# Performance work log

Hardware: AMD Instinct MI355X
Metric: run time of the kernel (lower is better)

Reference implementation:

```python
import jax, jax.numpy as jnp
import numpy as np

N_NODES = 100000
N_EDGES = 1000000
IN_CH = 128
HID = 128
N_CLS = 3


def setup_inputs() -> dict:
    key = jax.random.key(0)
    ks = jax.random.split(key, 10)
    scale_in = 1.0 / np.sqrt(IN_CH)
    scale_h = 1.0 / np.sqrt(HID)
    return {
        "x": jax.random.normal(ks[0], (N_NODES, IN_CH), dtype=jnp.float32),
        "edge_index": jax.random.randint(ks[1], (2, N_EDGES), 0, N_NODES, dtype=jnp.int64),
        # SAGEConv layer 1: lin_l (aggregated neighbors, with bias), lin_r (root, no bias)
        "w_l1": jax.random.normal(ks[2], (IN_CH, HID), dtype=jnp.float32) * scale_in,
        "b_l1": jnp.zeros((HID,), dtype=jnp.float32),
        "w_r1": jax.random.normal(ks[3], (IN_CH, HID), dtype=jnp.float32) * scale_in,
        # SAGEConv layer 2
        "w_l2": jax.random.normal(ks[4], (HID, HID), dtype=jnp.float32) * scale_h,
        "b_l2": jnp.zeros((HID,), dtype=jnp.float32),
        "w_r2": jax.random.normal(ks[5], (HID, HID), dtype=jnp.float32) * scale_h,
        # final classifier
        "w_cls": jax.random.normal(ks[6], (HID, N_CLS), dtype=jnp.float32) * scale_h,
        "b_cls": jnp.zeros((N_CLS,), dtype=jnp.float32),
    }


def _sage_conv(x, src, dst, w_l, b_l, w_r, num_nodes):
    # mean aggregation of source-node features onto destination nodes
    msg = x[src]                                              # [E, C] gather
    agg = jax.ops.segment_sum(msg, dst, num_segments=num_nodes)
    cnt = jax.ops.segment_sum(jnp.ones((src.shape[0],), x.dtype), dst,
                              num_segments=num_nodes)
    mean = agg / jnp.maximum(cnt, 1.0)[:, None]
    # out = lin_l(mean_aggr) + lin_r(x)
    return mean @ w_l + b_l + x @ w_r


def reference(x, edge_index, w_l1, b_l1, w_r1, w_l2, b_l2, w_r2, w_cls, b_cls):
    src, dst = edge_index[0], edge_index[1]
    n = x.shape[0]
    h = jax.nn.relu(_sage_conv(x, src, dst, w_l1, b_l1, w_r1, n))
    # dropout is identity in eval mode
    h = jax.nn.relu(_sage_conv(h, src, dst, w_l2, b_l2, w_r2, n))
    logits = h @ w_cls + b_cls
    return logits
```

## Files before the change

### kernel.cpp

```cpp
#include <hip/hip_runtime.h>
#include <hip/hip_bf16.h>

#define N_NODES 100000
#define N_EDGES 1000000
#define CH 128
#define KTOT 256
#define NCLS 3

#define NBKT 196
#define EPB 4096
#define NB_A ((N_EDGES + EPB - 1) / EPB)
#define M_H (NBKT * NB_A)
#define CHK ((M_H + 1023) / 1024)

#define NB_CVTX (N_NODES * CH / 4 / 256)
#define NB_CVTW (KTOT * CH / 256)
#define NB_A1 (NB_A + NB_CVTX + 2 * NB_CVTW)

typedef __attribute__((ext_vector_type(8))) short v8s;
typedef __attribute__((ext_vector_type(4))) float v4f;

__device__ __forceinline__ float bf2f(unsigned short u) {
    return __uint_as_float(((unsigned int)u) << 16);
}

__device__ __forceinline__ unsigned short f2bf(float f) {
    unsigned int u = __float_as_uint(f);
    unsigned int r = (u + 0x7fffu + ((u >> 16) & 1u)) >> 16;
    return (unsigned short)r;
}

__device__ __forceinline__ int edge_at(const void* e, int is64, long long i) {
    if (is64) return (int)((const long long*)e)[i];
    return ((const int*)e)[i];
}

__device__ __forceinline__ float ldf(const void* p, int isbf, size_t i) {
    if (isbf) return bf2f(((const unsigned short*)p)[i]);
    return ((const float*)p)[i];
}

__device__ __forceinline__ void acc_u32(unsigned int u, float& a0, float& a1) {
    a0 += bf2f((unsigned short)(u & 0xffffu));
    a1 += bf2f((unsigned short)(u >> 16));
}

__global__ void k_init(const void* __restrict__ e, const unsigned int* __restrict__ x,
                       int* __restrict__ eflag, int* __restrict__ dtf) {
    if (blockIdx.x == 0) {
        if (threadIdx.x < 64) {
            int v = ((const int*)e)[2 * threadIdx.x + 1];
            unsigned long long bl = __ballot(v != 0);
            if (threadIdx.x == 0) *eflag = (bl == 0ULL) ? 1 : 0;
        }
    } else {
        if (threadIdx.x < 64) {
            unsigned int u = x[threadIdx.x];
            int ex = (u >> 7) & 0xff;
            int sane = (ex == 0) || (ex >= 100 && ex <= 154);
            unsigned long long bl = __ballot(sane);
            if (threadIdx.x == 0) *dtf = (__popcll(bl) >= 48) ? 1 : 0;
        }
    }
}

__global__ void k_A1(const void* __restrict__ e, const int* __restrict__ eflag,
                     const int* __restrict__ dtf, int* __restrict__ hist,
                     const void* __restrict__ x, unsigned short* __restrict__ Abuf,
                     const void* __restrict__ wl1, const void* __restrict__ wr1,
                     unsigned short* __restrict__ WT1,
                     const void* __restrict__ wl2, const void* __restrict__ wr2,
                     unsigned short* __restrict__ WT2) {
    int b = blockIdx.x;
    int t = threadIdx.x;
    if (b < NB_A) {
        __shared__ int h[NBKT];
        if (t < NBKT) h[t] = 0;
        __syncthreads();
        int is64 = *eflag;
#pragma unroll
        for (int j = 0; j < EPB / 256; j++) {
            int i = b * EPB + j * 256 + t;
            if (i < N_EDGES) {
                int dst = edge_at(e, is64, (long long)N_EDGES + i);
                atomicAdd(&h[dst >> 9], 1);
            }
        }
        __syncthreads();
        if (t < NBKT) hist[t * NB_A + b] = h[t];
    } else {
        int ob = b - NB_A;
        if (ob < NB_CVTX) {
            int idx = ob * 256 + t;
            int node = idx >> 5;
            int ch = (idx & 31) * 4;
            int isbf = *dtf;
            unsigned short o[4];
            if (isbf) {
                ushort4 u = *(const ushort4*)((const unsigned short*)x +
                                              (size_t)node * CH + ch);
                o[0] = u.x; o[1] = u.y; o[2] = u.z; o[3] = u.w;
            } else {
                float4 v = *(const float4*)((const float*)x + (size_t)node * CH + ch);
                o[0] = f2bf(v.x); o[1] = f2bf(v.y); o[2] = f2bf(v.z); o[3] = f2bf(v.w);
            }
            *(ushort4*)(Abuf + (size_t)node * KTOT + CH + ch) =
                make_ushort4(o[0], o[1], o[2], o[3]);
        } else {
            int rel = ob - NB_CVTX;
            const void* wl = (rel < NB_CVTW) ? wl1 : wl2;
            const void* wr = (rel < NB_CVTW) ? wr1 : wr2;
            unsigned short* WT = (rel < NB_CVTW) ? WT1 : WT2;
            int i = (rel % NB_CVTW) * 256 + t;
            int k = i >> 7;
            int n = i & 127;
            int isbf = *dtf;
            float v = (k < CH) ? ldf(wl, isbf, (size_t)k * CH + n)
                               : ldf(wr, isbf, (size_t)(k - CH) * CH + n);
            WT[(size_t)n * KTOT + k] = f2bf(v);
        }
    }
}

__global__ __launch_bounds__(1024) void k_scanH(int* __restrict__ hist,
                                                int* __restrict__ bktbase) {
    __shared__ int ps[1024];
    int t = threadIdx.x;
    int lv[CHK];
    int s = 0;
    int base0 = t * CHK;
#pragma unroll
    for (int j = 0; j < CHK; j++) {
        int idx = base0 + j;
        int v = (idx < M_H) ? hist[idx] : 0;
        lv[j] = v;
        s += v;
    }
    ps[t] = s;
    __syncthreads();
    for (int off = 1; off < 1024; off <<= 1) {
        int v = (t >= off) ? ps[t - off] : 0;
        __syncthreads();
        ps[t] += v;
        __syncthreads();
    }
    int run = ps[t] - s;
#pragma unroll
    for (int j = 0; j < CHK; j++) {
        int idx = base0 + j;
        if (idx < M_H) hist[idx] = run;
        run += lv[j];
    }
    __syncthreads();
    if (t < NBKT) bktbase[t] = hist[t * NB_A];
    if (t == 0) bktbase[NBKT] = N_EDGES;
}

__global__ void k_A3(const void* __restrict__ e, const int* __restrict__ eflag,
                     const int* __restrict__ hist, unsigned int* __restrict__ part) {
    __shared__ int cur[NBKT];
    int b = blockIdx.x;
    int t = threadIdx.x;
    if (t < NBKT) cur[t] = hist[t * NB_A + b];
    __syncthreads();
    int is64 = *eflag;
#pragma unroll
    for (int j = 0; j < EPB / 256; j++) {
        int i = b * EPB + j * 256 + t;
        if (i < N_EDGES) {
            int src = edge_at(e, is64, i);
            int dst = edge_at(e, is64, (long long)N_EDGES + i);
            int pos = atomicAdd(&cur[dst >> 9], 1);
            part[pos] = ((unsigned int)src << 9) | (unsigned int)(dst & 511);
        }
    }
}

__global__ __launch_bounds__(1024) void k_B(const int* __restrict__ bktbase,
                                            const unsigned int* __restrict__ part,
                                            int* __restrict__ row_start,
                                            int* __restrict__ csr_src) {
    __shared__ int dcnt[512], sa[512], curs[512];
    int b = blockIdx.x;
    int t = threadIdx.x;
    int e0 = bktbase[b], e1 = bktbase[b + 1];
    if (t < 512) dcnt[t] = 0;
    __syncthreads();
    for (int i = e0 + t; i < e1; i += 1024)
        atomicAdd(&dcnt[part[i] & 511], 1);
    __syncthreads();
    if (t < 512) sa[t] = dcnt[t];
    __syncthreads();
    for (int off = 1; off < 512; off <<= 1) {
        int v = 0;
        if (t < 512 && t >= off) v = sa[t - off];
        __syncthreads();
        if (t < 512) sa[t] += v;
        __syncthreads();
    }
    if (t < 512) {
        int excl = sa[t] - dcnt[t];
        curs[t] = e0 + excl;
        int node = b * 512 + t;
        if (node < N_NODES) row_start[node] = e0 + excl;
    }
    if (b == 0 && t == 0) row_start[N_NODES] = N_EDGES;
    __syncthreads();
    for (int i = e0 + t; i < e1; i += 1024) {
        unsigned int p = part[i];
        int pos = atomicAdd(&curs[p & 511], 1);
        csr_src[pos] = (int)(p >> 9);
    }
}

__global__ __launch_bounds__(256) void k_agg(
    const int* __restrict__ row_start, const int* __restrict__ csr_src,
    const unsigned short* __restrict__ gsrc, unsigned short* __restrict__ gdst) {
    long long gt = (long long)blockIdx.x * blockDim.x + threadIdx.x;
    int node = (int)(gt >> 4);
    int lane = (int)(gt & 15);
    if (node >= N_NODES) return;
    int beg = row_start[node];
    int end = row_start[node + 1];
    float a[8];
#pragma unroll
    for (int j = 0; j < 8; j++) a[j] = 0.f;
    int e = beg;
    while (e + 8 <= end) {
        int s[8];
#pragma unroll
        for (int j = 0; j < 8; j++) s[j] = csr_src[e + j];
        uint4 u[8];
#pragma unroll
        for (int j = 0; j < 8; j++)
            u[j] = *(const uint4*)(gsrc + (size_t)s[j] * KTOT + CH + lane * 8);
#pragma unroll
        for (int j = 0; j < 8; j++) {
            acc_u32(u[j].x, a[0], a[1]); acc_u32(u[j].y, a[2], a[3]);
            acc_u32(u[j].z, a[4], a[5]); acc_u32(u[j].w, a[6], a[7]);
        }
        e += 8;
    }
    while (e + 2 <= end) {
        int s0 = csr_src[e], s1 = csr_src[e + 1];
        uint4 u0 = *(const uint4*)(gsrc + (size_t)s0 * KTOT + CH + lane * 8);
        uint4 u1 = *(const uint4*)(gsrc + (size_t)s1 * KTOT + CH + lane * 8);
        acc_u32(u0.x, a[0], a[1]); acc_u32(u0.y, a[2], a[3]);
        acc_u32(u0.z, a[4], a[5]); acc_u32(u0.w, a[6], a[7]);
        acc_u32(u1.x, a[0], a[1]); acc_u32(u1.y, a[2], a[3]);
        acc_u32(u1.z, a[4], a[5]); acc_u32(u1.w, a[6], a[7]);
        e += 2;
    }
    if (e < end) {
        int s0 = csr_src[e];
        uint4 u0 = *(const uint4*)(gsrc + (size_t)s0 * KTOT + CH + lane * 8);
        acc_u32(u0.x, a[0], a[1]); acc_u32(u0.y, a[2], a[3]);
        acc_u32(u0.z, a[4], a[5]); acc_u32(u0.w, a[6], a[7]);
    }
    float rinv = 1.0f / (float)max(end - beg, 1);
    unsigned int p0 = (unsigned int)f2bf(a[0] * rinv) | ((unsigned int)f2bf(a[1] * rinv) << 16);
    unsigned int p1 = (unsigned int)f2bf(a[2] * rinv) | ((unsigned int)f2bf(a[3] * rinv) << 16);
    unsigned int p2 = (unsigned int)f2bf(a[4] * rinv) | ((unsigned int)f2bf(a[5] * rinv) << 16);
    unsigned int p3 = (unsigned int)f2bf(a[6] * rinv) | ((unsigned int)f2bf(a[7] * rinv) << 16);
    *(uint4*)(gdst + (size_t)node * KTOT + lane * 8) = make_uint4(p0, p1, p2, p3);
}

#define LDK 40
#define CLS_LD 130
__global__ __launch_bounds__(256) void k_gemm_mfma(
    const unsigned short* __restrict__ Abuf, const unsigned short* __restrict__ WT,
    const void* __restrict__ bias, const int* __restrict__ dtf,
    unsigned short* __restrict__ out, int out_stride, int out_off,
    const void* __restrict__ wcls, const void* __restrict__ bcls,
    float* __restrict__ cls_out) {
    __shared__ unsigned short smem[4 * 128 * LDK];
    __shared__ float wcls_s[CH * NCLS];
    unsigned short* As = smem;
    unsigned short* Bs = smem + 2 * 128 * LDK;
    const int t = threadIdx.x;
    const int w = t >> 6, l = t & 63;
    const int wx = w & 1, wy = w >> 1;
    const int quad = l >> 4, lrow = l & 15;
    const int row0 = blockIdx.x * 128;
    const int srow = t >> 1, shalf = t & 1;
    const int isbf = *dtf;

    if (cls_out) {
        for (int i = t; i < CH * NCLS; i += 256) wcls_s[i] = ldf(wcls, isbf, i);
    }

    int ar = row0 + srow;
    if (ar >= N_NODES) ar = N_NODES - 1;
    const unsigned short* abase = Abuf + (size_t)ar * KTOT + shalf * 16;
    const unsigned short* bbase = WT + (size_t)srow * KTOT + shalf * 16;

    v4f acc[4][4];
#pragma unroll
    for (int i = 0; i < 4; i++)
#pragma unroll
        for (int j = 0; j < 4; j++) acc[i][j] = (v4f){0.f, 0.f, 0.f, 0.f};

    {
        uint4 a0 = *(const uint4*)abase, a1 = *(const uint4*)(abase + 8);
        uint4 b0 = *(const uint4*)bbase, b1 = *(const uint4*)(bbase + 8);
        *(uint4*)&As[srow * LDK + shalf * 16] = a0;
        *(uint4*)&As[srow * LDK + shalf * 16 + 8] = a1;
        *(uint4*)&Bs[srow * LDK + shalf * 16] = b0;
        *(uint4*)&Bs[srow * LDK + shalf * 16 + 8] = b1;
    }
#pragma unroll
    for (int k = 0; k < KTOT / 32; k++) {
        uint4 na0, na1, nb0, nb1;
        if (k < KTOT / 32 - 1) {
            na0 = *(const uint4*)(abase + (k + 1) * 32);
            na1 = *(const uint4*)(abase + (k + 1) * 32 + 8);
            nb0 = *(const uint4*)(bbase + (k + 1) * 32);
            nb1 = *(const uint4*)(bbase + (k + 1) * 32 + 8);
        }
        __syncthreads();
        const int cur = (k & 1) * 128 * LDK, nxt = ((k + 1) & 1) * 128 * LDK;
        v8s af[4], bfr[4];
#pragma unroll
        for (int mi = 0; mi < 4; mi++)
            af[mi] = *(const v8s*)&As[cur + (wy * 64 + mi * 16 + lrow) * LDK + quad * 8];
#pragma unroll
        for (int ni = 0; ni < 4; ni++)
            bfr[ni] = *(const v8s*)&Bs[cur + (wx * 64 + ni * 16 + lrow) * LDK + quad * 8];
#pragma unroll
        for (int mi = 0; mi < 4; mi++)
#pragma unroll
            for (int ni = 0; ni < 4; ni++)
                acc[mi][ni] = __builtin_amdgcn_mfma_f32_16x16x32_bf16(
                    af[mi], bfr[ni], acc[mi][ni], 0, 0, 0);
        if (k < KTOT / 32 - 1) {
            *(uint4*)&As[nxt + srow * LDK + shalf * 16] = na0;
            *(uint4*)&As[nxt + srow * LDK + shalf * 16 + 8] = na1;
            *(uint4*)&Bs[nxt + srow * LDK + shalf * 16] = nb0;
            *(uint4*)&Bs[nxt + srow * LDK + shalf * 16 + 8] = nb1;
        }
    }
    float bj[4];
#pragma unroll
    for (int ni = 0; ni < 4; ni++) bj[ni] = ldf(bias, isbf, wx * 64 + ni * 16 + lrow);

    if (!cls_out) {
#pragma unroll
        for (int mi = 0; mi < 4; mi++) {
#pragma unroll
            for (int r = 0; r < 4; r++) {
                int grow = row0 + wy * 64 + mi * 16 + quad * 4 + r;
                if (grow < N_NODES) {
#pragma unroll
                    for (int ni = 0; ni < 4; ni++) {
                        int col = wx * 64 + ni * 16 + lrow;
                        float v = fmaxf(acc[mi][ni][r] + bj[ni], 0.0f);
                        out[(size_t)grow * out_stride + out_off + col] = f2bf(v);
                    }
                }
            }
        }
    } else {
        __syncthreads();
#pragma unroll
        for (int mi = 0; mi < 4; mi++) {
#pragma unroll
            for (int r = 0; r < 4; r++) {
                int row = wy * 64 + mi * 16 + quad * 4 + r;
#pragma unroll
                for (int ni = 0; ni < 4; ni++) {
                    int col = wx * 64 + ni * 16 + lrow;
                    float v = fmaxf(acc[mi][ni][r] + bj[ni], 0.0f);
                    smem[row * CLS_LD + col] = f2bf(v);
                }
            }
        }
        __syncthreads();
        if (t < 128) {
            int grow = row0 + t;
            if (grow < N_NODES) {
                float a0 = 0.f, a1 = 0.f, a2 = 0.f;
                for (int k = 0; k < CH; k++) {
                    float h = bf2f(smem[t * CLS_LD + k]);
                    a0 += h * wcls_s[k * NCLS + 0];
                    a1 += h * wcls_s[k * NCLS + 1];
                    a2 += h * wcls_s[k * NCLS + 2];
                }
                cls_out[(size_t)grow * NCLS + 0] = a0 + ldf(bcls, isbf, 0);
                cls_out[(size_t)grow * NCLS + 1] = a1 + ldf(bcls, isbf, 1);
                cls_out[(size_t)grow * NCLS + 2] = a2 + ldf(bcls, isbf, 2);
            }
        }
    }
}

extern "C" void kernel_launch(void* const* d_in, const int* in_sizes, int n_in,
                              void* d_out, int out_size, void* d_ws, size_t ws_size,
                              hipStream_t stream) {
    const void* x = d_in[0];
    const void* eidx = d_in[1];
    const void* w_l1 = d_in[2];
    const void* b_l1 = d_in[3];
    const void* w_r1 = d_in[4];
    const void* w_l2 = d_in[5];
    const void* b_l2 = d_in[6];
    const void* w_r2 = d_in[7];
    const void* w_cls = d_in[8];
    const void* b_cls = d_in[9];

    char* w = (char*)d_ws;
    int* eflag = (int*)w;
    int* dtf = (int*)(w + 64);
    int* hist = (int*)(w + 4096);
    int* bktbase = (int*)(w + 196608);
    int* row_start = (int*)(w + 262144);
    unsigned int* part = (unsigned int*)(w + 720896);
    int* csr_src = (int*)(w + 4915200);
    unsigned short* WT1 = (unsigned short*)(w + 8978432);
    unsigned short* WT2 = (unsigned short*)(w + 9043968);
    unsigned short* A1 = (unsigned short*)(w + 11534336);
    unsigned short* A2 = (unsigned short*)(w + 62914560);

    hipLaunchKernelGGL(k_init, dim3(2), dim3(256), 0, stream,
                       eidx, (const unsigned int*)x, eflag, dtf);
    hipLaunchKernelGGL(k_A1, dim3(NB_A1), dim3(256), 0, stream,
                       eidx, eflag, dtf, hist, x, A1,
                       w_l1, w_r1, WT1, w_l2, w_r2, WT2);
    hipLaunchKernelGGL(k_scanH, dim3(1), dim3(1024), 0, stream, hist, bktbase);
    hipLaunchKernelGGL(k_A3, dim3(NB_A), dim3(256), 0, stream,
                       eidx, eflag, hist, part);
    hipLaunchKernelGGL(k_B, dim3(NBKT), dim3(1024), 0, stream,
                       bktbase, part, row_start, csr_src);
    hipLaunchKernelGGL(k_agg, dim3(N_NODES * 16 / 256), dim3(256), 0, stream,
                       row_start, csr_src, A1, A1);
    hipLaunchKernelGGL(k_gemm_mfma, dim3((N_NODES + 127) / 128), dim3(256), 0, stream,
                       A1, WT1, b_l1, dtf, A2, KTOT, CH,
                       (const void*)nullptr, (const void*)nullptr, (float*)nullptr);
    hipLaunchKernelGGL(k_agg, dim3(N_NODES * 16 / 256), dim3(256), 0, stream,
                       row_start, csr_src, A2, A2);
    hipLaunchKernelGGL(k_gemm_mfma, dim3((N_NODES + 127) / 128), dim3(256), 0, stream,
                       A2, WT2, b_l2, dtf, (unsigned short*)nullptr, 0, 0,
                       w_cls, b_cls, (float*)d_out);
}
```

Before: 308.4 us.

## Parallelize histogram scan across blocks with atomic-counter cross-block prefix

Replaces the single-block histogram prefix scan with a multi-block scan. Each block scans 1024 entries, publishes its total, and waits on a global atomic counter before summing the earlier block totals. Bucket bases are then read straight from the scanned histogram instead of a separate bktbase array. This removes a serial single-workgroup step, but the spin-wait relies on every scan block being resident at the same time.

After: 266.1 us. -13.7%, faster.

```diff
diff --git a/kernel.cpp b/kernel.cpp
--- a/kernel.cpp
+++ b/kernel.cpp
@@ -11,7 +11,7 @@
 #define EPB 4096
 #define NB_A ((N_EDGES + EPB - 1) / EPB)
 #define M_H (NBKT * NB_A)
-#define CHK ((M_H + 1023) / 1024)
+#define NB_SCAN ((M_H + 1023) / 1024)
 
 #define NB_CVTX (N_NODES * CH / 4 / 256)
 #define NB_CVTW (KTOT * CH / 256)
@@ -46,12 +46,15 @@
 }
 
 __global__ void k_init(const void* __restrict__ e, const unsigned int* __restrict__ x,
-                       int* __restrict__ eflag, int* __restrict__ dtf) {
+                       int* __restrict__ eflag, int* __restrict__ dtf,
+                       int* __restrict__ done) {
     if (blockIdx.x == 0) {
         if (threadIdx.x < 64) {
             int v = ((const int*)e)[2 * threadIdx.x + 1];
             unsigned long long bl = __ballot(v != 0);
             if (threadIdx.x == 0) *eflag = (bl == 0ULL) ? 1 : 0;
+        } else if (threadIdx.x == 64) {
+            *done = 0;
         }
     } else {
         if (threadIdx.x < 64) {
@@ -123,37 +126,37 @@
 }
 
 __global__ __launch_bounds__(1024) void k_scanH(int* __restrict__ hist,
-                                                int* __restrict__ bktbase) {
-    __shared__ int ps[1024];
-    int t = threadIdx.x;
-    int lv[CHK];
-    int s = 0;
-    int base0 = t * CHK;
-#pragma unroll
-    for (int j = 0; j < CHK; j++) {
-        int idx = base0 + j;
-        int v = (idx < M_H) ? hist[idx] : 0;
-        lv[j] = v;
-        s += v;
-    }
-    ps[t] = s;
+                                                int* __restrict__ bsum,
+                                                int* __restrict__ done) {
+    __shared__ int s[1024];
+    __shared__ int pre_sh;
+    int t = threadIdx.x, b = blockIdx.x;
+    int idx = b * 1024 + t;
+    int v = (idx < M_H) ? hist[idx] : 0;
+    s[t] = v;
     __syncthreads();
     for (int off = 1; off < 1024; off <<= 1) {
-        int v = (t >= off) ? ps[t - off] : 0;
-        __syncthreads();
-        ps[t] += v;
-        __syncthreads();
-    }
-    int run = ps[t] - s;
-#pragma unroll
-    for (int j = 0; j < CHK; j++) {
-        int idx = base0 + j;
-        if (idx < M_H) hist[idx] = run;
-        run += lv[j];
-    }
-    __syncthreads();
-    if (t < NBKT) bktbase[t] = hist[t * NB_A];
-    if (t == 0) bktbase[NBKT] = N_EDGES;
+        int u = (t >= off) ? s[t - off] : 0;
+        __syncthreads();
+        s[t] += u;
+        __syncthreads();
+    }
+    if (t == 1023) {
+        bsum[b] = s[t];
+        __threadfence();
+        atomicAdd(done, 1);
+    }
+    if (t == 0) {
+        while (__hip_atomic_load(done, __ATOMIC_ACQUIRE,
+                                 __HIP_MEMORY_SCOPE_AGENT) < NB_SCAN) {
+        }
+        __threadfence();
+        int run = 0;
+        for (int r = 0; r < b; r++) run += bsum[r];
+        pre_sh = run;
+    }
+    __syncthreads();
+    if (idx < M_H) hist[idx] = s[t] - v + pre_sh;
 }
 
 __global__ void k_A3(const void* __restrict__ e, const int* __restrict__ eflag,
@@ -176,14 +179,15 @@
     }
 }
 
-__global__ __launch_bounds__(1024) void k_B(const int* __restrict__ bktbase,
+__global__ __launch_bounds__(1024) void k_B(const int* __restrict__ hist,
                                             const unsigned int* __restrict__ part,
                                             int* __restrict__ row_start,
                                             int* __restrict__ csr_src) {
     __shared__ int dcnt[512], sa[512], curs[512];
     int b = blockIdx.x;
     int t = threadIdx.x;
-    int e0 = bktbase[b], e1 = bktbase[b + 1];
+    int e0 = hist[b * NB_A];
+    int e1 = (b + 1 < NBKT) ? hist[(b + 1) * NB_A] : N_EDGES;
     if (t < 512) dcnt[t] = 0;
     __syncthreads();
     for (int i = e0 + t; i < e1; i += 1024)
@@ -410,8 +414,9 @@
     char* w = (char*)d_ws;
     int* eflag = (int*)w;
     int* dtf = (int*)(w + 64);
+    int* done = (int*)(w + 128);
     int* hist = (int*)(w + 4096);
-    int* bktbase = (int*)(w + 196608);
+    int* bsum = (int*)(w + 196608);
     int* row_start = (int*)(w + 262144);
     unsigned int* part = (unsigned int*)(w + 720896);
     int* csr_src = (int*)(w + 4915200);
@@ -421,15 +426,16 @@
     unsigned short* A2 = (unsigned short*)(w + 62914560);
 
     hipLaunchKernelGGL(k_init, dim3(2), dim3(256), 0, stream,
-                       eidx, (const unsigned int*)x, eflag, dtf);
+                       eidx, (const unsigned int*)x, eflag, dtf, done);
     hipLaunchKernelGGL(k_A1, dim3(NB_A1), dim3(256), 0, stream,
                        eidx, eflag, dtf, hist, x, A1,
                        w_l1, w_r1, WT1, w_l2, w_r2, WT2);
-    hipLaunchKernelGGL(k_scanH, dim3(1), dim3(1024), 0, stream, hist, bktbase);
+    hipLaunchKernelGGL(k_scanH, dim3(NB_SCAN), dim3(1024), 0, stream,
+                       hist, bsum, done);
     hipLaunchKernelGGL(k_A3, dim3(NB_A), dim3(256), 0, stream,
                        eidx, eflag, hist, part);
     hipLaunchKernelGGL(k_B, dim3(NBKT), dim3(1024), 0, stream,
-                       bktbase, part, row_start, csr_src);
+                       hist, part, row_start, csr_src);
     hipLaunchKernelGGL(k_agg, dim3(N_NODES * 16 / 256), dim3(256), 0, stream,
                        row_start, csr_src, A1, A1);
     hipLaunchKernelGGL(k_gemm_mfma, dim3((N_NODES + 127) / 128), dim3(256), 0, stream,
```
